# Kernel optimization log

Measured on AMD Instinct MI355X. Metric: run time of the kernel, lower is better.

## Reference

```python
import jax, jax.numpy as jnp
import numpy as np

N, E, F_NODE, F_EDGE, H, L, G = 4096, 12288, 64, 16, 128, 4, 256
BN_EPS = 1e-5


def setup_inputs() -> dict:
    key = jax.random.key(0)
    ks = jax.random.split(key, 20)
    s = lambda k, shape, fan: jax.random.normal(k, shape, jnp.float32) * (1.0 / np.sqrt(fan))
    inp = {
        'x': jax.random.normal(ks[0], (N, F_NODE), jnp.float32),
        'edge_index': jax.random.randint(ks[1], (2, E), 0, N, dtype=jnp.int64),
        'edge_attr': jax.random.normal(ks[2], (E, F_EDGE), jnp.float32),
        'batch': jnp.sort(jax.random.randint(ks[3], (N,), 0, G, dtype=jnp.int64)),
        # node encoder
        'node_w': s(ks[4], (F_NODE, H), F_NODE),
        'node_b': jnp.zeros((H,), jnp.float32),
        # per-layer edge MLP: edge_feat -> 128 -> H*H
        'e1_w': s(ks[5], (L, F_EDGE, 128), F_EDGE),
        'e1_b': jnp.zeros((L, 128), jnp.float32),
        'e2_w': s(ks[6], (L, 128, H * H), 128) * 0.1,
        'e2_b': jnp.zeros((L, H * H), jnp.float32),
        # NNConv root weight + bias
        'root_w': s(ks[7], (L, H, H), H),
        'conv_b': jnp.zeros((L, H), jnp.float32),
        # batchnorm affine
        'bn_g': jnp.ones((L, H), jnp.float32),
        'bn_b': jnp.zeros((L, H), jnp.float32),
        # head
        'head_w1': s(ks[8], (H, H), H),
        'head_b1': jnp.zeros((H,), jnp.float32),
        'head_w2': s(ks[9], (H, 1), H),
        'head_b2': jnp.zeros((1,), jnp.float32),
    }
    return inp


def reference(x, edge_index, edge_attr, batch, node_w, node_b, e1_w, e1_b,
              e2_w, e2_b, root_w, conv_b, bn_g, bn_b, head_w1, head_b1,
              head_w2, head_b2):
    src, dst = edge_index[0], edge_index[1]
    h = x @ node_w + node_b  # [N,H]
    # in-degree for mean aggregation
    deg = jax.ops.segment_sum(jnp.ones((E,), h.dtype), dst, num_segments=N)
    inv_deg = jnp.where(deg > 0, 1.0 / jnp.maximum(deg, 1.0), 0.0)[:, None]
    for l in range(L):
        # edge MLP -> per-edge [H,H] weight
        e = jax.nn.relu(edge_attr @ e1_w[l] + e1_b[l])            # [E,128]
        W_e = (e @ e2_w[l] + e2_b[l]).reshape(E, H, H)            # [E,H,H]
        msg = jnp.einsum('eh,eho->eo', h[src], W_e)               # [E,H]
        agg = jax.ops.segment_sum(msg, dst, num_segments=N) * inv_deg
        out = agg + h @ root_w[l] + conv_b[l]
        # batchnorm (training-mode batch stats, biased var as in torch)
        mu = out.mean(0)
        var = out.var(0)
        out = (out - mu) * jax.lax.rsqrt(var + BN_EPS) * bn_g[l] + bn_b[l]
        h = h + jax.nn.relu(out)  # dropout disabled (eval)
    # global mean pool over graphs
    cnt = jax.ops.segment_sum(jnp.ones((N,), h.dtype), batch, num_segments=G)
    pooled = jax.ops.segment_sum(h, batch, num_segments=G) / jnp.maximum(cnt, 1.0)[:, None]
    y = jax.nn.relu(pooled @ head_w1 + head_b1) @ head_w2 + head_b2
    return y.squeeze(-1)  # [G]
```

## Files before the change

### kernel.cpp

```cpp
#include <hip/hip_runtime.h>

#define N_NODES 4096
#define E_TOT   12288
#define F_NODE  64
#define F_EDGE  16
#define HDIM    128
#define NLAYER  4
#define NGRAPH  256

typedef _Float16 half8 __attribute__((ext_vector_type(8)));
typedef float    f32x4 __attribute__((ext_vector_type(4)));

__global__ void k_prep_w2(const float* __restrict__ e2w, const float* __restrict__ e2b,
                          _Float16* __restrict__ W2F)
{
    int t = blockIdx.x * 256 + threadIdx.x;
    const int PER_L = 129 * 16384;
    if (t >= NLAYER * PER_L) return;
    int l   = t / PER_L;
    int r   = t - l * PER_L;
    int k   = r >> 14;
    int rem = r & 16383;
    int chunk = rem >> 9;
    int lane  = (rem >> 3) & 63;
    int j     = rem & 7;
    int hc = chunk >> 3, ot = chunk & 7;
    int h  = hc * 32 + (lane >> 4) * 8 + j;
    int o  = ot * 16 + (lane & 15);
    float v;
    if (k < 128) v = e2w[((size_t)(l * 128 + k)) * 16384 + h * 128 + o];
    else         v = e2b[(size_t)l * 16384 + h * 128 + o];
    W2F[t] = (_Float16)v;
}

__global__ __launch_bounds__(128)
void k_node_enc(const float* __restrict__ x, const float* __restrict__ nw,
                const float* __restrict__ nb, float* __restrict__ h,
                _Float16* __restrict__ hf)
{
    __shared__ float xl[F_NODE];
    int n = blockIdx.x, o = threadIdx.x;
    if (o < F_NODE) xl[o] = x[(size_t)n * F_NODE + o];
    __syncthreads();
    float acc = nb[o];
#pragma unroll 8
    for (int f = 0; f < F_NODE; ++f) acc += xl[f] * nw[f * HDIM + o];
    h [(size_t)n * HDIM + o] = acc;
    hf[(size_t)n * HDIM + o] = (_Float16)acc;
}

__global__ void k_deg(const int* __restrict__ dst, int* __restrict__ deg)
{
    int e = blockIdx.x * 256 + threadIdx.x;
    if (e < E_TOT) atomicAdd(&deg[dst[e]], 1);
}

__global__ void k_invd(const int* __restrict__ deg, float* __restrict__ invd)
{
    int n = blockIdx.x * 256 + threadIdx.x;
    if (n < N_NODES) invd[n] = deg[n] > 0 ? 1.0f / (float)deg[n] : 0.0f;
}

#define EF_STRIDE 136
__global__ __launch_bounds__(128)
void k_edge_mlp(const float* __restrict__ ea, const float* __restrict__ w1,
                const float* __restrict__ b1, _Float16* __restrict__ efg)
{
    __shared__ float al[F_EDGE];
    int e = blockIdx.x, j = threadIdx.x;
    if (j < F_EDGE) al[j] = ea[(size_t)e * F_EDGE + j];
    __syncthreads();
    float acc = b1[j];
#pragma unroll
    for (int f = 0; f < F_EDGE; ++f) acc += al[f] * w1[f * HDIM + j];
    acc = fmaxf(acc, 0.f);
    efg[(size_t)e * EF_STRIDE + j] = (_Float16)acc;
    if (j == 0) efg[(size_t)e * EF_STRIDE + 128] = (_Float16)1.0f;
}

__global__ __launch_bounds__(512, 2)
void k_msg(const _Float16* __restrict__ W2L,
           const _Float16* __restrict__ efg,
           const _Float16* __restrict__ hf,
           const int* __restrict__ srcIdx,
           const int* __restrict__ dstIdx,
           float* __restrict__ agg)
{
    __shared__ _Float16 Bb[3][16384];
    __shared__ _Float16 efs[256][40];

    const int tid  = threadIdx.x;
    const int lane = tid & 63;
    const int w    = tid >> 6;
    const int rq   = w >> 1;
    const int ch   = w & 1;
    const int lhi  = lane >> 4;
    const int llo  = lane & 15;

    const int bx    = blockIdx.x;
    const int ks    = (bx >> 1) & 3;
    const int tile  = (bx >> 3) * 2 + (bx & 1);
    const int e0    = tile * 256;
    const int kbase = (129 * ks) >> 2;
    const int kcnt  = ((129 * (ks + 1)) >> 2) - kbase;

    {
        int r = tid >> 1, h2 = tid & 1;
        const half8* sp = (const half8*)(efg + (size_t)(e0 + r) * EF_STRIDE + kbase);
        half8* dp = (half8*)&efs[r][0];
        if (h2 == 0) { dp[0] = sp[0]; dp[1] = sp[1]; dp[2] = sp[2]; }
        else         { dp[3] = sp[3]; dp[4] = sp[4]; }
    }

    half8 hs[4][4];
#pragma unroll
    for (int rf = 0; rf < 4; ++rf) {
        int s = srcIdx[e0 + rq * 64 + rf * 16 + llo];
        const _Float16* hp = hf + (size_t)s * HDIM + lhi * 8;
#pragma unroll
        for (int hc = 0; hc < 4; ++hc)
            hs[rf][hc] = *(const half8*)(hp + hc * 32);
    }

    asm volatile("s_waitcnt vmcnt(0) lgkmcnt(0)" ::: "memory");

    auto STAGE = [&](int kg, int buf) {
        const _Float16* g = W2L + (size_t)kg * 16384 + w * 2048 + lane * 8;
        _Float16* lp = &Bb[buf][w * 2048];
#pragma unroll
        for (int i = 0; i < 4; ++i)
            __builtin_amdgcn_global_load_lds(
                (const __attribute__((address_space(1))) void*)(g + i * 512),
                (__attribute__((address_space(3))) void*)(lp + i * 512), 16, 0, 0);
    };

    STAGE(kbase + 0, 0);
    STAGE(kbase + 1, 1);

    f32x4 acc[4][4];
#pragma unroll
    for (int rf = 0; rf < 4; ++rf)
#pragma unroll
        for (int cf = 0; cf < 4; ++cf)
#pragma unroll
            for (int d = 0; d < 4; ++d) acc[rf][cf][d] = 0.f;

    int cur = 0, stg = 2;
    for (int kk = 0; kk < kcnt; ++kk) {
        asm volatile("" ::: "memory");
        __builtin_amdgcn_s_barrier();
        asm volatile("" ::: "memory");
        if (kk + 2 < kcnt) {
            STAGE(kbase + kk + 2, stg);
            asm volatile("s_waitcnt vmcnt(8)" ::: "memory");
        } else if (kk + 1 < kcnt) {
            asm volatile("s_waitcnt vmcnt(4)" ::: "memory");
        } else {
            asm volatile("s_waitcnt vmcnt(0)" ::: "memory");
        }
        asm volatile("" ::: "memory");
        __builtin_amdgcn_s_barrier();
        asm volatile("" ::: "memory");

        _Float16 efv[4];
        const _Float16* erow = &efs[rq * 64 + llo][kk];
#pragma unroll
        for (int rf = 0; rf < 4; ++rf) efv[rf] = erow[rf * 16 * 40];

        const _Float16* bb = &Bb[cur][ch * 2048 + lane * 8];
#pragma unroll
        for (int hc = 0; hc < 4; ++hc) {
            half8 bfr[4];
#pragma unroll
            for (int cf = 0; cf < 4; ++cf)
                bfr[cf] = *(const half8*)(bb + hc * 4096 + cf * 512);
#pragma unroll
            for (int rf = 0; rf < 4; ++rf) {
                half8 av = hs[rf][hc] * efv[rf];
#pragma unroll
                for (int cf = 0; cf < 4; ++cf)
                    acc[rf][cf] = __builtin_amdgcn_mfma_f32_16x16x32_f16(
                        av, bfr[cf], acc[rf][cf], 0, 0, 0);
            }
        }
        cur = cur == 2 ? 0 : cur + 1;
        stg = stg == 2 ? 0 : stg + 1;
    }

#pragma unroll
    for (int rf = 0; rf < 4; ++rf) {
#pragma unroll
        for (int r = 0; r < 4; ++r) {
            int row = rq * 64 + rf * 16 + lhi * 4 + r;
            int d   = dstIdx[e0 + row];
#pragma unroll
            for (int cf = 0; cf < 4; ++cf) {
                int o = ch * 64 + cf * 16 + llo;
                atomicAdd(&agg[(size_t)d * HDIM + o], acc[rf][cf][r]);
            }
        }
    }
}

__global__ __launch_bounds__(128)
void k_out(const float* __restrict__ agg, const float* __restrict__ invd,
           const float* __restrict__ h, const float* __restrict__ rw,
           const float* __restrict__ cb, float* __restrict__ outb)
{
    __shared__ float hl[16][HDIM];
    int n0 = blockIdx.x * 16, o = threadIdx.x;
    for (int r = 0; r < 16; ++r) hl[r][o] = h[(size_t)(n0 + r) * HDIM + o];
    __syncthreads();
    float acc[16];
    float cbv = cb[o];
#pragma unroll
    for (int r = 0; r < 16; ++r)
        acc[r] = agg[(size_t)(n0 + r) * HDIM + o] * invd[n0 + r] + cbv;
    for (int hh = 0; hh < HDIM; ++hh) {
        float wv = rw[hh * HDIM + o];
#pragma unroll
        for (int r = 0; r < 16; ++r) acc[r] += hl[r][hh] * wv;
    }
#pragma unroll
    for (int r = 0; r < 16; ++r) outb[(size_t)(n0 + r) * HDIM + o] = acc[r];
}

__global__ __launch_bounds__(256)
void k_bn_stats(const float* __restrict__ outb, float* __restrict__ mu,
                float* __restrict__ rsig)
{
    __shared__ float s1[256], s2[256];
    int c = blockIdx.x, t = threadIdx.x;
    float a = 0.f, b = 0.f;
    for (int n = t; n < N_NODES; n += 256) {
        float v = outb[(size_t)n * HDIM + c];
        a += v; b += v * v;
    }
    s1[t] = a; s2[t] = b;
    __syncthreads();
    for (int s = 128; s > 0; s >>= 1) {
        if (t < s) { s1[t] += s1[t + s]; s2[t] += s2[t + s]; }
        __syncthreads();
    }
    if (t == 0) {
        float m   = s1[0] / (float)N_NODES;
        float var = s2[0] / (float)N_NODES - m * m;
        mu[c]   = m;
        rsig[c] = rsqrtf(var + 1e-5f);
    }
}

__global__ void k_bn_apply(const float* __restrict__ outb, const float* __restrict__ mu,
                           const float* __restrict__ rsig, const float* __restrict__ g,
                           const float* __restrict__ b, float* __restrict__ h,
                           _Float16* __restrict__ hf)
{
    int i = blockIdx.x * 256 + threadIdx.x;
    int o = i & (HDIM - 1);
    float v  = (outb[i] - mu[o]) * rsig[o] * g[o] + b[o];
    float hn = h[i] + fmaxf(v, 0.f);
    h[i]  = hn;
    hf[i] = (_Float16)hn;
}

__global__ __launch_bounds__(128)
void k_pool(const float* __restrict__ h, const int* __restrict__ batch,
            float* __restrict__ pooled, int* __restrict__ cnt)
{
    int n = blockIdx.x, c = threadIdx.x;
    int g = batch[n];
    atomicAdd(&pooled[(size_t)g * HDIM + c], h[(size_t)n * HDIM + c]);
    if (c == 0) atomicAdd(&cnt[g], 1);
}

__global__ __launch_bounds__(128)
void k_head(const float* __restrict__ pooled, const int* __restrict__ cnt,
            const float* __restrict__ w1, const float* __restrict__ b1,
            const float* __restrict__ w2, const float* __restrict__ b2,
            float* __restrict__ y)
{
    __shared__ float pl[HDIM];
    __shared__ float red[HDIM];
    int g = blockIdx.x, o = threadIdx.x;
    float ic = 1.0f / (float)max(cnt[g], 1);
    pl[o] = pooled[(size_t)g * HDIM + o] * ic;
    __syncthreads();
    float t = b1[o];
#pragma unroll 8
    for (int hh = 0; hh < HDIM; ++hh) t += pl[hh] * w1[hh * HDIM + o];
    t = fmaxf(t, 0.f);
    red[o] = t * w2[o];
    __syncthreads();
    for (int s = 64; s > 0; s >>= 1) {
        if (o < s) red[o] += red[o + s];
        __syncthreads();
    }
    if (o == 0) y[g] = red[0] + b2[0];
}

extern "C" void kernel_launch(void* const* d_in, const int* in_sizes, int n_in,
                              void* d_out, int out_size, void* d_ws, size_t ws_size,
                              hipStream_t stream)
{
    const float* x      = (const float*)d_in[0];
    const int*   ei     = (const int*)  d_in[1];
    const float* ea     = (const float*)d_in[2];
    const int*   batch  = (const int*)  d_in[3];
    const float* node_w = (const float*)d_in[4];
    const float* node_b = (const float*)d_in[5];
    const float* e1w    = (const float*)d_in[6];
    const float* e1b    = (const float*)d_in[7];
    const float* e2w    = (const float*)d_in[8];
    const float* e2b    = (const float*)d_in[9];
    const float* rw     = (const float*)d_in[10];
    const float* cb     = (const float*)d_in[11];
    const float* bng    = (const float*)d_in[12];
    const float* bnb    = (const float*)d_in[13];
    const float* hw1    = (const float*)d_in[14];
    const float* hb1    = (const float*)d_in[15];
    const float* hw2    = (const float*)d_in[16];
    const float* hb2    = (const float*)d_in[17];
    float* y = (float*)d_out;

    char* ws = (char*)d_ws;
    _Float16* W2F  = (_Float16*)ws; ws += 16908288;
    float*    h    = (float*)ws;    ws += 2097152;
    _Float16* hf   = (_Float16*)ws; ws += 1048576;
    _Float16* efg  = (_Float16*)ws; ws += 3342336;
    float*    agg  = (float*)ws;    ws += 2097152;
    float*    outb = (float*)ws;    ws += 2097152;
    int*      deg  = (int*)ws;      ws += 16384;
    float*    invd = (float*)ws;    ws += 16384;
    float*    mu   = (float*)ws;    ws += 512;
    float*    rsig = (float*)ws;    ws += 512;
    float*    pooled = (float*)ws;  ws += 131072;
    int*      cnt  = (int*)ws;      ws += 1024;

    const int* src = ei;
    const int* dst = ei + E_TOT;

    k_prep_w2<<<33024, 256, 0, stream>>>(e2w, e2b, W2F);
    k_node_enc<<<N_NODES, 128, 0, stream>>>(x, node_w, node_b, h, hf);
    hipMemsetAsync(deg, 0, N_NODES * sizeof(int), stream);
    k_deg<<<(E_TOT + 255) / 256, 256, 0, stream>>>(dst, deg);
    k_invd<<<(N_NODES + 255) / 256, 256, 0, stream>>>(deg, invd);

    for (int l = 0; l < NLAYER; ++l) {
        k_edge_mlp<<<E_TOT, 128, 0, stream>>>(ea, e1w + l * F_EDGE * HDIM,
                                              e1b + l * HDIM, efg);
        hipMemsetAsync(agg, 0, (size_t)N_NODES * HDIM * sizeof(float), stream);
        k_msg<<<(E_TOT / 256) * 4, 512, 0, stream>>>(W2F + (size_t)l * 129 * 16384,
                                                     efg, hf, src, dst, agg);
        k_out<<<N_NODES / 16, 128, 0, stream>>>(agg, invd, h,
                                                rw + l * HDIM * HDIM,
                                                cb + l * HDIM, outb);
        k_bn_stats<<<HDIM, 256, 0, stream>>>(outb, mu, rsig);
        k_bn_apply<<<(N_NODES * HDIM) / 256, 256, 0, stream>>>(
            outb, mu, rsig, bng + l * HDIM, bnb + l * HDIM, h, hf);
    }

    hipMemsetAsync(pooled, 0, (size_t)NGRAPH * HDIM * sizeof(float), stream);
    hipMemsetAsync(cnt, 0, NGRAPH * sizeof(int), stream);
    k_pool<<<N_NODES, 128, 0, stream>>>(h, batch, pooled, cnt);
    k_head<<<NGRAPH, 128, 0, stream>>>(pooled, cnt, hw1, hb1, hw2, hb2, y);
}
```

Before: 494.1 us.

## Shrink msg tiles to 96 edges, double-buffer, and split atomics per k-slice

The message kernel now processes 96-edge tiles instead of 256, with 8 waves laid out as 2 row groups by 4 column groups. The W2 staging drops from triple to double buffering so each block uses less LDS and four blocks can fit per CU. Each of the four k-split slices now atomically adds into its own partial aggregation buffer, and k_out sums the four partials, which reduces atomic contention. In exchange the partial buffers take four times the memory and memset traffic, and each block reuses the staged W2 across fewer edges, so total W2 loads rise about 2.7x.

```diff
diff --git a/kernel.cpp b/kernel.cpp
--- a/kernel.cpp
+++ b/kernel.cpp
@@ -78,44 +78,44 @@
     if (j == 0) efg[(size_t)e * EF_STRIDE + 128] = (_Float16)1.0f;
 }
 
-__global__ __launch_bounds__(512, 2)
+#define BM 96
+__global__ __launch_bounds__(512, 4)
 void k_msg(const _Float16* __restrict__ W2L,
            const _Float16* __restrict__ efg,
            const _Float16* __restrict__ hf,
            const int* __restrict__ srcIdx,
            const int* __restrict__ dstIdx,
-           float* __restrict__ agg)
-{
-    __shared__ _Float16 Bb[3][16384];
-    __shared__ _Float16 efs[256][40];
+           float* __restrict__ agg4)
+{
+    __shared__ _Float16 Bb[2][16384];
+    __shared__ _Float16 efs[BM][40];
 
     const int tid  = threadIdx.x;
     const int lane = tid & 63;
     const int w    = tid >> 6;
-    const int rq   = w >> 1;
-    const int ch   = w & 1;
+    const int rq   = w >> 2;
+    const int ch   = w & 3;
     const int lhi  = lane >> 4;
     const int llo  = lane & 15;
 
     const int bx    = blockIdx.x;
     const int ks    = (bx >> 1) & 3;
-    const int tile  = (bx >> 3) * 2 + (bx & 1);
-    const int e0    = tile * 256;
+    const int tile  = (bx & 1) + (bx >> 3) * 2;
+    const int e0    = tile * BM;
     const int kbase = (129 * ks) >> 2;
     const int kcnt  = ((129 * (ks + 1)) >> 2) - kbase;
-
-    {
-        int r = tid >> 1, h2 = tid & 1;
-        const half8* sp = (const half8*)(efg + (size_t)(e0 + r) * EF_STRIDE + kbase);
-        half8* dp = (half8*)&efs[r][0];
-        if (h2 == 0) { dp[0] = sp[0]; dp[1] = sp[1]; dp[2] = sp[2]; }
-        else         { dp[3] = sp[3]; dp[4] = sp[4]; }
-    }
-
-    half8 hs[4][4];
-#pragma unroll
-    for (int rf = 0; rf < 4; ++rf) {
-        int s = srcIdx[e0 + rq * 64 + rf * 16 + llo];
+    float* agg = agg4 + (size_t)ks * N_NODES * HDIM;
+
+    if (tid < BM * 5) {
+        int r = tid / 5, c = tid - r * 5;
+        *(half8*)&efs[r][c * 8] =
+            *(const half8*)(efg + (size_t)(e0 + r) * EF_STRIDE + kbase + c * 8);
+    }
+
+    half8 hs[3][4];
+#pragma unroll
+    for (int rf = 0; rf < 3; ++rf) {
+        int s = srcIdx[e0 + rq * 48 + rf * 16 + llo];
         const _Float16* hp = hf + (size_t)s * HDIM + lhi * 8;
 #pragma unroll
         for (int hc = 0; hc < 4; ++hc)
@@ -135,25 +135,22 @@
     };
 
     STAGE(kbase + 0, 0);
-    STAGE(kbase + 1, 1);
-
-    f32x4 acc[4][4];
-#pragma unroll
-    for (int rf = 0; rf < 4; ++rf)
-#pragma unroll
-        for (int cf = 0; cf < 4; ++cf)
+
+    f32x4 acc[3][2];
+#pragma unroll
+    for (int rf = 0; rf < 3; ++rf)
+#pragma unroll
+        for (int cf = 0; cf < 2; ++cf)
 #pragma unroll
             for (int d = 0; d < 4; ++d) acc[rf][cf][d] = 0.f;
 
-    int cur = 0, stg = 2;
     for (int kk = 0; kk < kcnt; ++kk) {
+        const int cur = kk & 1;
         asm volatile("" ::: "memory");
         __builtin_amdgcn_s_barrier();
         asm volatile("" ::: "memory");
-        if (kk + 2 < kcnt) {
-            STAGE(kbase + kk + 2, stg);
-            asm volatile("s_waitcnt vmcnt(8)" ::: "memory");
-        } else if (kk + 1 < kcnt) {
+        if (kk + 1 < kcnt) {
+            STAGE(kbase + kk + 1, cur ^ 1);
             asm volatile("s_waitcnt vmcnt(4)" ::: "memory");
         } else {
             asm volatile("s_waitcnt vmcnt(0)" ::: "memory");
@@ -162,40 +159,39 @@
         __builtin_amdgcn_s_barrier();
         asm volatile("" ::: "memory");
 
-        _Float16 efv[4];
-        const _Float16* erow = &efs[rq * 64 + llo][kk];
-#pragma unroll
-        for (int rf = 0; rf < 4; ++rf) efv[rf] = erow[rf * 16 * 40];
-
-        const _Float16* bb = &Bb[cur][ch * 2048 + lane * 8];
+        _Float16 efv[3];
+#pragma unroll
+        for (int rf = 0; rf < 3; ++rf) efv[rf] = efs[rq * 48 + rf * 16 + llo][kk];
+
+        const _Float16* bb = &Bb[cur][ch * 1024 + lane * 8];
+        __builtin_amdgcn_s_setprio(1);
 #pragma unroll
         for (int hc = 0; hc < 4; ++hc) {
-            half8 bfr[4];
-#pragma unroll
-            for (int cf = 0; cf < 4; ++cf)
+            half8 bfr[2];
+#pragma unroll
+            for (int cf = 0; cf < 2; ++cf)
                 bfr[cf] = *(const half8*)(bb + hc * 4096 + cf * 512);
 #pragma unroll
-            for (int rf = 0; rf < 4; ++rf) {
+            for (int rf = 0; rf < 3; ++rf) {
                 half8 av = hs[rf][hc] * efv[rf];
 #pragma unroll
-                for (int cf = 0; cf < 4; ++cf)
+                for (int cf = 0; cf < 2; ++cf)
                     acc[rf][cf] = __builtin_amdgcn_mfma_f32_16x16x32_f16(
                         av, bfr[cf], acc[rf][cf], 0, 0, 0);
             }
         }
-        cur = cur == 2 ? 0 : cur + 1;
-        stg = stg == 2 ? 0 : stg + 1;
-    }
-
-#pragma unroll
-    for (int rf = 0; rf < 4; ++rf) {
+        __builtin_amdgcn_s_setprio(0);
+    }
+
+#pragma unroll
+    for (int rf = 0; rf < 3; ++rf) {
 #pragma unroll
         for (int r = 0; r < 4; ++r) {
-            int row = rq * 64 + rf * 16 + lhi * 4 + r;
+            int row = rq * 48 + rf * 16 + lhi * 4 + r;
             int d   = dstIdx[e0 + row];
 #pragma unroll
-            for (int cf = 0; cf < 4; ++cf) {
-                int o = ch * 64 + cf * 16 + llo;
+            for (int cf = 0; cf < 2; ++cf) {
+                int o = ch * 32 + cf * 16 + llo;
                 atomicAdd(&agg[(size_t)d * HDIM + o], acc[rf][cf][r]);
             }
         }
@@ -203,7 +199,7 @@
 }
 
 __global__ __launch_bounds__(128)
-void k_out(const float* __restrict__ agg, const float* __restrict__ invd,
+void k_out(const float* __restrict__ agg4, const float* __restrict__ invd,
            const float* __restrict__ h, const float* __restrict__ rw,
            const float* __restrict__ cb, float* __restrict__ outb)
 {
@@ -214,8 +210,13 @@
     float acc[16];
     float cbv = cb[o];
 #pragma unroll
-    for (int r = 0; r < 16; ++r)
-        acc[r] = agg[(size_t)(n0 + r) * HDIM + o] * invd[n0 + r] + cbv;
+    for (int r = 0; r < 16; ++r) {
+        float s = 0.f;
+#pragma unroll
+        for (int p = 0; p < 4; ++p)
+            s += agg4[(size_t)p * N_NODES * HDIM + (size_t)(n0 + r) * HDIM + o];
+        acc[r] = s * invd[n0 + r] + cbv;
+    }
     for (int hh = 0; hh < HDIM; ++hh) {
         float wv = rw[hh * HDIM + o];
 #pragma unroll
@@ -327,7 +328,7 @@
     float*    h    = (float*)ws;    ws += 2097152;
     _Float16* hf   = (_Float16*)ws; ws += 1048576;
     _Float16* efg  = (_Float16*)ws; ws += 3342336;
-    float*    agg  = (float*)ws;    ws += 2097152;
+    float*    agg4 = (float*)ws;    ws += 8388608;
     float*    outb = (float*)ws;    ws += 2097152;
     int*      deg  = (int*)ws;      ws += 16384;
     float*    invd = (float*)ws;    ws += 16384;
@@ -348,10 +349,10 @@
     for (int l = 0; l < NLAYER; ++l) {
         k_edge_mlp<<<E_TOT, 128, 0, stream>>>(ea, e1w + l * F_EDGE * HDIM,
                                               e1b + l * HDIM, efg);
-        hipMemsetAsync(agg, 0, (size_t)N_NODES * HDIM * sizeof(float), stream);
-        k_msg<<<(E_TOT / 256) * 4, 512, 0, stream>>>(W2F + (size_t)l * 129 * 16384,
-                                                     efg, hf, src, dst, agg);
-        k_out<<<N_NODES / 16, 128, 0, stream>>>(agg, invd, h,
+        hipMemsetAsync(agg4, 0, (size_t)4 * N_NODES * HDIM * sizeof(float), stream);
+        k_msg<<<(E_TOT / BM) * 4, 512, 0, stream>>>(W2F + (size_t)l * 129 * 16384,
+                                                    efg, hf, src, dst, agg4);
+        k_out<<<N_NODES / 16, 128, 0, stream>>>(agg4, invd, h,
                                                 rw + l * HDIM * HDIM,
                                                 cb + l * HDIM, outb);
         k_bn_stats<<<HDIM, 256, 0, stream>>>(outb, mu, rsig);
```

Result: faster. 471.3 us (-4.6%).
